# Performance work log

Hardware: AMD Instinct MI355X
Metric: run time of the kernel (lower is better)

The kernel has to match this reference:

```python
import math
import jax, jax.numpy as jnp
import numpy as np

B, S, D = 64, 729, 64  # S = (32*14//16 - 1)**2

def setup_inputs() -> dict:
    key = jax.random.key(0)
    kq, kk, kv, km = jax.random.split(key, 4)
    return {
        "query": jax.random.normal(kq, (B, S, D), dtype=jnp.float32),
        "key": jax.random.normal(kk, (B, S, D), dtype=jnp.float32),
        "value": jax.random.normal(kv, (B, S, D), dtype=jnp.float32),
        "mask": jax.random.randint(km, (B, S, S), 0, 2, dtype=jnp.int32),
    }

def reference(query, key, value, mask):
    dk = query.shape[-1]
    # [B,S,S] scores
    scores = jnp.einsum('bqd,bkd->bqk', query, key) / math.sqrt(dk)
    scores = jnp.where(mask == 0, jnp.float32(-1e9), scores)
    attention = jnp.tanh(scores)  # args.activation == 'tanh'
    # ignore_diag == 1: zero the diagonal of each [S,S] attention map
    eye = jnp.eye(attention.shape[-1], dtype=attention.dtype)
    attention = attention * (1.0 - eye)
    out = jnp.einsum('bqk,bkd->bqd', attention, value)
    return (out, attention)
```

## Files before the change

kernel.cpp:

```cpp
#include <hip/hip_runtime.h>

#define BATCH 64
#define SEQ 729
#define DIM 64
#define NT 12
#define STRB 72
#define STRW 68

typedef __attribute__((ext_vector_type(8))) short bf16x8;
typedef __attribute__((ext_vector_type(4))) float f32x4;
typedef int   i32x4a __attribute__((ext_vector_type(4), aligned(4)));
typedef float f32x4a __attribute__((ext_vector_type(4), aligned(4)));

__device__ __forceinline__ unsigned short f2bf(float f) {
    unsigned int u = __float_as_uint(f);
    u += 0x7fffu + ((u >> 16) & 1u);
    return (unsigned short)(u >> 16);
}

__device__ __forceinline__ unsigned long long pack4bf(float a, float b, float c, float d) {
    return (unsigned long long)f2bf(a)
         | ((unsigned long long)f2bf(b) << 16)
         | ((unsigned long long)f2bf(c) << 32)
         | ((unsigned long long)f2bf(d) << 48);
}

__device__ __forceinline__ float fast_tanh(float x) {
    float e = __builtin_amdgcn_exp2f(x * 2.88539008177792681f);
    return 1.0f - 2.0f * __builtin_amdgcn_rcpf(e + 1.0f);
}

__global__ __launch_bounds__(256, 3) void attn_kernel(
    const float* __restrict__ Qg, const float* __restrict__ Kg,
    const float* __restrict__ Vg, const int* __restrict__ Mg,
    float* __restrict__ Og, float* __restrict__ Ag)
{
    __shared__ unsigned short Ks[64 * STRB];
    __shared__ unsigned short Vs[64 * STRB];
    __shared__ unsigned short Qs[64 * STRB];
    __shared__ float Pf[64 * STRW];
    int* Mint = (int*)Pf;

    const int tid = threadIdx.x;
    const int q0  = blockIdx.x * 64;
    const int b   = blockIdx.y;

    const float* Qb = Qg + (size_t)b * SEQ * DIM;
    const float* Kb = Kg + (size_t)b * SEQ * DIM;
    const float* Vb = Vg + (size_t)b * SEQ * DIM;
    const int*   Mb = Mg + (size_t)b * SEQ * SEQ;
    float* Ob = Og + (size_t)b * SEQ * DIM;
    float* Ab = Ag + (size_t)b * SEQ * SEQ;

    const int lane = tid & 63;
    const int quad = lane >> 4;
    const int l15  = lane & 15;
    const int qrow = (tid >> 6) * 16;

    const int rr = tid >> 4;
    const int cc = (tid & 15) * 4;
    const int vd0 = (tid & 15) * 4;
    const int vk0 = (tid >> 4) * 4;
    const int prow = qrow + (lane >> 4);
    const int pcol = (lane & 15) * 4;

    float4 kr[4], vr[4];
    i32x4a mr[4];

    auto load_k = [&](int k0n) {
        #pragma unroll
        for (int i = 0; i < 4; ++i) {
            int gk = k0n + rr + 16 * i;
            kr[i] = (gk < SEQ) ? *(const float4*)(Kb + gk * DIM + cc)
                               : float4{0, 0, 0, 0};
        }
    };
    auto load_v = [&](int k0n) {
        #pragma unroll
        for (int i = 0; i < 4; ++i) {
            int gk = k0n + vk0 + i;
            vr[i] = (gk < SEQ) ? *(const float4*)(Vb + gk * DIM + vd0)
                               : float4{0, 0, 0, 0};
        }
    };
    auto load_mask = [&](int k0n) {
        #pragma unroll
        for (int i = 0; i < 4; ++i) {
            int gq = q0 + prow + 4 * i;
            int gk = k0n + pcol;
            if (gq < SEQ && gk + 3 < SEQ) {
                mr[i] = *(const i32x4a*)(Mb + (size_t)gq * SEQ + gk);
            } else if (gq < SEQ) {
                i32x4a t;
                #pragma unroll
                for (int e = 0; e < 4; ++e)
                    t[e] = (gk + e < SEQ) ? Mb[(size_t)gq * SEQ + gk + e] : 0;
                mr[i] = t;
            } else {
                mr[i] = i32x4a{0, 0, 0, 0};
            }
        }
    };
    auto drain_mask = [&]() {
        #pragma unroll
        for (int i = 0; i < 4; ++i)
            *(i32x4a*)&Mint[(prow + 4 * i) * STRW + pcol] = mr[i];
    };
    auto drain_kv = [&]() {
        #pragma unroll
        for (int i = 0; i < 4; ++i)
            *(unsigned long long*)&Ks[(rr + 16 * i) * STRB + cc] =
                pack4bf(kr[i].x, kr[i].y, kr[i].z, kr[i].w);
        #pragma unroll
        for (int j = 0; j < 4; ++j) {
            float v0 = j==0?vr[0].x:j==1?vr[0].y:j==2?vr[0].z:vr[0].w;
            float v1 = j==0?vr[1].x:j==1?vr[1].y:j==2?vr[1].z:vr[1].w;
            float v2 = j==0?vr[2].x:j==1?vr[2].y:j==2?vr[2].z:vr[2].w;
            float v3 = j==0?vr[3].x:j==1?vr[3].y:j==2?vr[3].z:vr[3].w;
            *(unsigned long long*)&Vs[(vd0 + j) * STRB + vk0] = pack4bf(v0, v1, v2, v3);
        }
    };

    #pragma unroll
    for (int i = 0; i < 4; ++i) {
        int gq = q0 + rr + 16 * i;
        float4 x = (gq < SEQ) ? *(const float4*)(Qb + gq * DIM + cc)
                              : float4{0, 0, 0, 0};
        *(unsigned long long*)&Qs[(rr + 16 * i) * STRB + cc] = pack4bf(x.x, x.y, x.z, x.w);
    }
    __syncthreads();

    const bf16x8 aq0 = *(const bf16x8*)&Qs[(qrow + l15) * STRB + quad * 8];
    const bf16x8 aq1 = *(const bf16x8*)&Qs[(qrow + l15) * STRB + 32 + quad * 8];

    load_k(0); load_v(0); load_mask(0);

    f32x4 oacc[4];
    #pragma unroll
    for (int dt = 0; dt < 4; ++dt) {
        oacc[dt][0]=0.f; oacc[dt][1]=0.f; oacc[dt][2]=0.f; oacc[dt][3]=0.f;
    }

    for (int kt = 0; kt < NT; ++kt) {
        const int k0 = kt * 64;

        __syncthreads();
        drain_mask();
        drain_kv();
        __syncthreads();

        if (kt + 1 < NT) {
            load_k(k0 + 64); load_v(k0 + 64); load_mask(k0 + 64);
        }

        f32x4 sacc[4];
        #pragma unroll
        for (int nt2 = 0; nt2 < 4; ++nt2) {
            bf16x8 bk0 = *(const bf16x8*)&Ks[(nt2 * 16 + l15) * STRB + quad * 8];
            bf16x8 bk1 = *(const bf16x8*)&Ks[(nt2 * 16 + l15) * STRB + 32 + quad * 8];
            f32x4 c; c[0]=0.f; c[1]=0.f; c[2]=0.f; c[3]=0.f;
            c = __builtin_amdgcn_mfma_f32_16x16x32_bf16(aq0, bk0, c, 0, 0, 0);
            c = __builtin_amdgcn_mfma_f32_16x16x32_bf16(aq1, bk1, c, 0, 0, 0);
            sacc[nt2] = c;
        }

        #pragma unroll
        for (int nt2 = 0; nt2 < 4; ++nt2) {
            int col = nt2 * 16 + l15;
            int gk  = k0 + col;
            #pragma unroll
            for (int r = 0; r < 4; ++r) {
                int qloc = qrow + quad * 4 + r;
                int gq = q0 + qloc;
                int m = Mint[qloc * STRW + col];
                float sv = sacc[nt2][r] * 0.125f;
                bool msk = (m == 0);
                float p = fast_tanh(msk ? -1e9f : sv);
                if (msk) p = -1.0f;
                if (gq == gk) p = 0.0f;
                if (gq >= SEQ || gk >= SEQ) p = 0.0f;
                Pf[qloc * STRW + col] = p;
                Qs[qloc * STRB + col] = f2bf(p);
            }
        }

        #pragma unroll
        for (int i = 0; i < 4; ++i) {
            int row = prow + 4 * i;
            int gq  = q0 + row;
            int gk  = k0 + pcol;
            f32x4 pv = *(const f32x4*)&Pf[row * STRW + pcol];
            if (gq < SEQ) {
                if (gk + 3 < SEQ) {
                    *(f32x4a*)(Ab + (size_t)gq * SEQ + gk) = pv;
                } else {
                    #pragma unroll
                    for (int e = 0; e < 4; ++e)
                        if (gk + e < SEQ) Ab[(size_t)gq * SEQ + gk + e] = pv[e];
                }
            }
        }

        const bf16x8 ap0 = *(const bf16x8*)&Qs[(qrow + l15) * STRB + quad * 8];
        const bf16x8 ap1 = *(const bf16x8*)&Qs[(qrow + l15) * STRB + 32 + quad * 8];
        #pragma unroll
        for (int dt = 0; dt < 4; ++dt) {
            bf16x8 bv0 = *(const bf16x8*)&Vs[(dt * 16 + l15) * STRB + quad * 8];
            bf16x8 bv1 = *(const bf16x8*)&Vs[(dt * 16 + l15) * STRB + 32 + quad * 8];
            oacc[dt] = __builtin_amdgcn_mfma_f32_16x16x32_bf16(ap0, bv0, oacc[dt], 0, 0, 0);
            oacc[dt] = __builtin_amdgcn_mfma_f32_16x16x32_bf16(ap1, bv1, oacc[dt], 0, 0, 0);
        }
    }

    #pragma unroll
    for (int dt = 0; dt < 4; ++dt)
        #pragma unroll
        for (int r = 0; r < 4; ++r)
            Pf[(qrow + quad * 4 + r) * STRW + dt * 16 + l15] = oacc[dt][r];
    #pragma unroll
    for (int i = 0; i < 4; ++i) {
        int row = prow + 4 * i;
        int gq  = q0 + row;
        f32x4 ov = *(const f32x4*)&Pf[row * STRW + pcol];
        if (gq < SEQ) *(f32x4*)(Ob + (size_t)gq * DIM + pcol) = ov;
    }
}

extern "C" void kernel_launch(void* const* d_in, const int* in_sizes, int n_in,
                              void* d_out, int out_size, void* d_ws, size_t ws_size,
                              hipStream_t stream) {
    const float* Q = (const float*)d_in[0];
    const float* K = (const float*)d_in[1];
    const float* V = (const float*)d_in[2];
    const int*   M = (const int*)d_in[3];
    float* Out  = (float*)d_out;
    float* Attn = Out + (size_t)BATCH * SEQ * DIM;
    dim3 grid(NT, BATCH);
    attn_kernel<<<grid, 256, 0, stream>>>(Q, K, V, M, Out, Attn);
}
```

Measured before the change: 326.7 us.

## Double-buffer K/V/mask tile prefetch in registers and repad V LDS stride

Replaces the single register staging set with two tile buffers (TA, TB), so loads for tile kt+2 are in flight while tile kt is computed. The Q load is also overlapped with the first two tile prefetches. The V shared-memory stride changes from 72 to 66 to reduce bank conflicts on the transposed V stores. The hand-written bf16 rounding is swapped for HIP bf16 conversion intrinsics. The second register tile raises register pressure under the 3-wave launch bound. The odd V stride makes 8- and 16-byte LDS accesses misaligned, which could be split or slowed.

```diff
diff --git a/kernel.cpp b/kernel.cpp
--- a/kernel.cpp
+++ b/kernel.cpp
@@ -1,44 +1,51 @@
 #include <hip/hip_runtime.h>
+#include <hip/hip_bf16.h>
 
 #define BATCH 64
 #define SEQ 729
 #define DIM 64
 #define NT 12
-#define STRB 72
-#define STRW 68
+#define KSTR 72
+#define VSTR 66
+#define PSTR 68
 
 typedef __attribute__((ext_vector_type(8))) short bf16x8;
 typedef __attribute__((ext_vector_type(4))) float f32x4;
 typedef int   i32x4a __attribute__((ext_vector_type(4), aligned(4)));
 typedef float f32x4a __attribute__((ext_vector_type(4), aligned(4)));
 
-__device__ __forceinline__ unsigned short f2bf(float f) {
-    unsigned int u = __float_as_uint(f);
-    u += 0x7fffu + ((u >> 16) & 1u);
-    return (unsigned short)(u >> 16);
-}
-
-__device__ __forceinline__ unsigned long long pack4bf(float a, float b, float c, float d) {
-    return (unsigned long long)f2bf(a)
-         | ((unsigned long long)f2bf(b) << 16)
-         | ((unsigned long long)f2bf(c) << 32)
-         | ((unsigned long long)f2bf(d) << 48);
+__device__ __forceinline__ void st4bf(unsigned short* p, float a, float b, float c, float d) {
+    __hip_bfloat162 lo = __float22bfloat162_rn(float2{a, b});
+    __hip_bfloat162 hi = __float22bfloat162_rn(float2{c, d});
+    unsigned int ulo = *(unsigned int*)&lo;
+    unsigned int uhi = *(unsigned int*)&hi;
+    *(unsigned long long*)p = (unsigned long long)ulo | ((unsigned long long)uhi << 32);
+}
+__device__ __forceinline__ unsigned short f2bf1(float f) {
+    __hip_bfloat16 h = __float2bfloat16(f);
+    return *(unsigned short*)&h;
 }
 
 __device__ __forceinline__ float fast_tanh(float x) {
     float e = __builtin_amdgcn_exp2f(x * 2.88539008177792681f);
     return 1.0f - 2.0f * __builtin_amdgcn_rcpf(e + 1.0f);
 }
+
+struct Tile {
+    float4 kr[4];
+    float4 vr[4];
+    i32x4a mr[4];
+};
 
 __global__ __launch_bounds__(256, 3) void attn_kernel(
     const float* __restrict__ Qg, const float* __restrict__ Kg,
     const float* __restrict__ Vg, const int* __restrict__ Mg,
     float* __restrict__ Og, float* __restrict__ Ag)
 {
-    __shared__ unsigned short Ks[64 * STRB];
-    __shared__ unsigned short Vs[64 * STRB];
-    __shared__ unsigned short Qs[64 * STRB];
-    __shared__ float Pf[64 * STRW];
+    __shared__ unsigned short Ks[64 * KSTR];
+    __shared__ unsigned short Vs[64 * VSTR];
+    __shared__ unsigned short Qs[64 * KSTR];
+    __shared__ float Pf[64 * PSTR];
     int* Mint = (int*)Pf;
 
     const int tid = threadIdx.x;
@@ -64,76 +71,74 @@
     const int prow = qrow + (lane >> 4);
     const int pcol = (lane & 15) * 4;
 
-    float4 kr[4], vr[4];
-    i32x4a mr[4];
-
-    auto load_k = [&](int k0n) {
+    auto load_tile = [&](Tile& T, int kt) {
+        const int k0n = kt * 64;
         #pragma unroll
         for (int i = 0; i < 4; ++i) {
             int gk = k0n + rr + 16 * i;
-            kr[i] = (gk < SEQ) ? *(const float4*)(Kb + gk * DIM + cc)
-                               : float4{0, 0, 0, 0};
-        }
-    };
-    auto load_v = [&](int k0n) {
+            T.kr[i] = (gk < SEQ) ? *(const float4*)(Kb + gk * DIM + cc)
+                                 : float4{0, 0, 0, 0};
+        }
         #pragma unroll
         for (int i = 0; i < 4; ++i) {
             int gk = k0n + vk0 + i;
-            vr[i] = (gk < SEQ) ? *(const float4*)(Vb + gk * DIM + vd0)
-                               : float4{0, 0, 0, 0};
-        }
-    };
-    auto load_mask = [&](int k0n) {
+            T.vr[i] = (gk < SEQ) ? *(const float4*)(Vb + gk * DIM + vd0)
+                                 : float4{0, 0, 0, 0};
+        }
         #pragma unroll
         for (int i = 0; i < 4; ++i) {
             int gq = q0 + prow + 4 * i;
             int gk = k0n + pcol;
             if (gq < SEQ && gk + 3 < SEQ) {
-                mr[i] = *(const i32x4a*)(Mb + (size_t)gq * SEQ + gk);
+                T.mr[i] = *(const i32x4a*)(Mb + (size_t)gq * SEQ + gk);
             } else if (gq < SEQ) {
                 i32x4a t;
                 #pragma unroll
                 for (int e = 0; e < 4; ++e)
                     t[e] = (gk + e < SEQ) ? Mb[(size_t)gq * SEQ + gk + e] : 0;
-                mr[i] = t;
+                T.mr[i] = t;
             } else {
-                mr[i] = i32x4a{0, 0, 0, 0};
+                T.mr[i] = i32x4a{0, 0, 0, 0};
             }
         }
     };
-    auto drain_mask = [&]() {
+
+    auto drain_tile = [&](Tile& T) {
         #pragma unroll
         for (int i = 0; i < 4; ++i)
-            *(i32x4a*)&Mint[(prow + 4 * i) * STRW + pcol] = mr[i];
+            st4bf(&Ks[(rr + 16 * i) * KSTR + cc],
+                  T.kr[i].x, T.kr[i].y, T.kr[i].z, T.kr[i].w);
+        #pragma unroll
+        for (int j = 0; j < 4; ++j) {
+            float v0 = j==0?T.vr[0].x:j==1?T.vr[0].y:j==2?T.vr[0].z:T.vr[0].w;
+            float v1 = j==0?T.vr[1].x:j==1?T.vr[1].y:j==2?T.vr[1].z:T.vr[1].w;
+            float v2 = j==0?T.vr[2].x:j==1?T.vr[2].y:j==2?T.vr[2].z:T.vr[2].w;
+            float v3 = j==0?T.vr[3].x:j==1?T.vr[3].y:j==2?T.vr[3].z:T.vr[3].w;
+            st4bf(&Vs[(vd0 + j) * VSTR + vk0], v0, v1, v2, v3);
+        }
+        #pragma unroll
+        for (int i = 0; i < 4; ++i)
+            *(i32x4a*)&Mint[(prow + 4 * i) * PSTR + pcol] = T.mr[i];
     };
-    auto drain_kv = [&]() {
-        #pragma unroll
-        for (int i = 0; i < 4; ++i)
-            *(unsigned long long*)&Ks[(rr + 16 * i) * STRB + cc] =
-                pack4bf(kr[i].x, kr[i].y, kr[i].z, kr[i].w);
-        #pragma unroll
-        for (int j = 0; j < 4; ++j) {
-            float v0 = j==0?vr[0].x:j==1?vr[0].y:j==2?vr[0].z:vr[0].w;
-            float v1 = j==0?vr[1].x:j==1?vr[1].y:j==2?vr[1].z:vr[1].w;
-            float v2 = j==0?vr[2].x:j==1?vr[2].y:j==2?vr[2].z:vr[2].w;
-            float v3 = j==0?vr[3].x:j==1?vr[3].y:j==2?vr[3].z:vr[3].w;
-            *(unsigned long long*)&Vs[(vd0 + j) * STRB + vk0] = pack4bf(v0, v1, v2, v3);
-        }
-    };
-
+
+    float4 qx[4];
     #pragma unroll
     for (int i = 0; i < 4; ++i) {
         int gq = q0 + rr + 16 * i;
-        float4 x = (gq < SEQ) ? *(const float4*)(Qb + gq * DIM + cc)
-                              : float4{0, 0, 0, 0};
-        *(unsigned long long*)&Qs[(rr + 16 * i) * STRB + cc] = pack4bf(x.x, x.y, x.z, x.w);
-    }
+        qx[i] = (gq < SEQ) ? *(const float4*)(Qb + gq * DIM + cc)
+                           : float4{0, 0, 0, 0};
+    }
+    Tile TA, TB;
+    load_tile(TA, 0);
+    load_tile(TB, 1);
+
+    #pragma unroll
+    for (int i = 0; i < 4; ++i)
+        st4bf(&Qs[(rr + 16 * i) * KSTR + cc], qx[i].x, qx[i].y, qx[i].z, qx[i].w);
     __syncthreads();
 
-    const bf16x8 aq0 = *(const bf16x8*)&Qs[(qrow + l15) * STRB + quad * 8];
-    const bf16x8 aq1 = *(const bf16x8*)&Qs[(qrow + l15) * STRB + 32 + quad * 8];
-
-    load_k(0); load_v(0); load_mask(0);
+    const bf16x8 aq0 = *(const bf16x8*)&Qs[(qrow + l15) * KSTR + quad * 8];
+    const bf16x8 aq1 = *(const bf16x8*)&Qs[(qrow + l15) * KSTR + 32 + quad * 8];
 
     f32x4 oacc[4];
     #pragma unroll
@@ -141,29 +146,18 @@
         oacc[dt][0]=0.f; oacc[dt][1]=0.f; oacc[dt][2]=0.f; oacc[dt][3]=0.f;
     }
 
-    for (int kt = 0; kt < NT; ++kt) {
+    auto compute_tile = [&](int kt) {
         const int k0 = kt * 64;
-
-        __syncthreads();
-        drain_mask();
-        drain_kv();
-        __syncthreads();
-
-        if (kt + 1 < NT) {
-            load_k(k0 + 64); load_v(k0 + 64); load_mask(k0 + 64);
-        }
-
         f32x4 sacc[4];
         #pragma unroll
         for (int nt2 = 0; nt2 < 4; ++nt2) {
-            bf16x8 bk0 = *(const bf16x8*)&Ks[(nt2 * 16 + l15) * STRB + quad * 8];
-            bf16x8 bk1 = *(const bf16x8*)&Ks[(nt2 * 16 + l15) * STRB + 32 + quad * 8];
+            bf16x8 bk0 = *(const bf16x8*)&Ks[(nt2 * 16 + l15) * KSTR + quad * 8];
+            bf16x8 bk1 = *(const bf16x8*)&Ks[(nt2 * 16 + l15) * KSTR + 32 + quad * 8];
             f32x4 c; c[0]=0.f; c[1]=0.f; c[2]=0.f; c[3]=0.f;
             c = __builtin_amdgcn_mfma_f32_16x16x32_bf16(aq0, bk0, c, 0, 0, 0);
             c = __builtin_amdgcn_mfma_f32_16x16x32_bf16(aq1, bk1, c, 0, 0, 0);
             sacc[nt2] = c;
         }
-
         #pragma unroll
         for (int nt2 = 0; nt2 < 4; ++nt2) {
             int col = nt2 * 16 + l15;
@@ -172,24 +166,23 @@
             for (int r = 0; r < 4; ++r) {
                 int qloc = qrow + quad * 4 + r;
                 int gq = q0 + qloc;
-                int m = Mint[qloc * STRW + col];
+                int m = Mint[qloc * PSTR + col];
                 float sv = sacc[nt2][r] * 0.125f;
                 bool msk = (m == 0);
                 float p = fast_tanh(msk ? -1e9f : sv);
                 if (msk) p = -1.0f;
                 if (gq == gk) p = 0.0f;
                 if (gq >= SEQ || gk >= SEQ) p = 0.0f;
-                Pf[qloc * STRW + col] = p;
-                Qs[qloc * STRB + col] = f2bf(p);
+                Pf[qloc * PSTR + col] = p;
+                Qs[qloc * KSTR + col] = f2bf1(p);
             }
         }
-
         #pragma unroll
         for (int i = 0; i < 4; ++i) {
             int row = prow + 4 * i;
             int gq  = q0 + row;
             int gk  = k0 + pcol;
-            f32x4 pv = *(const f32x4*)&Pf[row * STRW + pcol];
+            f32x4 pv = *(const f32x4*)&Pf[row * PSTR + pcol];
             if (gq < SEQ) {
                 if (gk + 3 < SEQ) {
                     *(f32x4a*)(Ab + (size_t)gq * SEQ + gk) = pv;
@@ -200,28 +193,41 @@
                 }
             }
         }
-
-        const bf16x8 ap0 = *(const bf16x8*)&Qs[(qrow + l15) * STRB + quad * 8];
-        const bf16x8 ap1 = *(const bf16x8*)&Qs[(qrow + l15) * STRB + 32 + quad * 8];
+        const bf16x8 ap0 = *(const bf16x8*)&Qs[(qrow + l15) * KSTR + quad * 8];
+        const bf16x8 ap1 = *(const bf16x8*)&Qs[(qrow + l15) * KSTR + 32 + quad * 8];
         #pragma unroll
         for (int dt = 0; dt < 4; ++dt) {
-            bf16x8 bv0 = *(const bf16x8*)&Vs[(dt * 16 + l15) * STRB + quad * 8];
-            bf16x8 bv1 = *(const bf16x8*)&Vs[(dt * 16 + l15) * STRB + 32 + quad * 8];
+            bf16x8 bv0 = *(const bf16x8*)&Vs[(dt * 16 + l15) * VSTR + quad * 8];
+            bf16x8 bv1 = *(const bf16x8*)&Vs[(dt * 16 + l15) * VSTR + 32 + quad * 8];
             oacc[dt] = __builtin_amdgcn_mfma_f32_16x16x32_bf16(ap0, bv0, oacc[dt], 0, 0, 0);
             oacc[dt] = __builtin_amdgcn_mfma_f32_16x16x32_bf16(ap1, bv1, oacc[dt], 0, 0, 0);
         }
+    };
+
+    for (int kt = 0; kt < NT; kt += 2) {
+        __syncthreads();
+        drain_tile(TA);
+        __syncthreads();
+        if (kt + 2 < NT) load_tile(TA, kt + 2);
+        compute_tile(kt);
+
+        __syncthreads();
+        drain_tile(TB);
+        __syncthreads();
+        if (kt + 3 < NT) load_tile(TB, kt + 3);
+        compute_tile(kt + 1);
     }
 
     #pragma unroll
     for (int dt = 0; dt < 4; ++dt)
         #pragma unroll
         for (int r = 0; r < 4; ++r)
-            Pf[(qrow + quad * 4 + r) * STRW + dt * 16 + l15] = oacc[dt][r];
+            Pf[(qrow + quad * 4 + r) * PSTR + dt * 16 + l15] = oacc[dt][r];
     #pragma unroll
     for (int i = 0; i < 4; ++i) {
         int row = prow + 4 * i;
         int gq  = q0 + row;
-        f32x4 ov = *(const f32x4*)&Pf[row * STRW + pcol];
+        f32x4 ov = *(const f32x4*)&Pf[row * PSTR + pcol];
         if (gq < SEQ) *(f32x4*)(Ob + (size_t)gq * DIM + pcol) = ov;
     }
 }
```

Result: slower. 414.9 us (+27.0%).
